# Optimization experiments

Measured on AMD Instinct MI355X. Metric: run time of the kernel, lower is better.

Reference implementation:

```python
import jax, jax.numpy as jnp
import numpy as np

HID = 1024
HEADS = 16
HEAD_DIM = HID // HEADS


def setup_inputs() -> dict:
    key = jax.random.key(0)
    ks = jax.random.split(key, 12)
    B, S = 4, 2048
    scale = 0.02
    return {
        "query": jax.random.normal(ks[0], (B, S, HID), jnp.float32),
        "key": jax.random.normal(ks[1], (B, S, HID), jnp.float32),
        "value": jax.random.normal(ks[2], (B, S, HID), jnp.float32),
        "wq": jax.random.normal(ks[3], (HID, HID), jnp.float32) * scale,
        "bq": jnp.zeros((HID,), jnp.float32),
        "wk": jax.random.normal(ks[4], (HID, HID), jnp.float32) * scale,
        "bk": jnp.zeros((HID,), jnp.float32),
        "wv": jax.random.normal(ks[5], (HID, HID), jnp.float32) * scale,
        "bv": jnp.zeros((HID,), jnp.float32),
        "wf": jax.random.normal(ks[6], (HID, HID), jnp.float32) * scale,
        "bf": jnp.zeros((HID,), jnp.float32),
    }


def reference(query, key, value, wq, bq, wk, bk, wv, bv, wf, bf):
    B, S, _ = query.shape
    # torch Linear: y = x @ W.T + b
    Q = (query @ wq.T + bq).reshape(B, S, HEADS, HEAD_DIM).transpose(0, 2, 1, 3)
    K = (key @ wk.T + bk).reshape(B, S, HEADS, HEAD_DIM).transpose(0, 2, 1, 3)
    V = (value @ wv.T + bv).reshape(B, S, HEADS, HEAD_DIM).transpose(0, 2, 1, 3)
    scale = jnp.sqrt(jnp.float32(HEAD_DIM))
    energy = jnp.einsum('bhqd,bhkd->bhqk', Q, K) / scale  # [B,H,S,S]
    attention = jax.nn.softmax(energy, axis=-1)  # dropout p=0 -> identity
    x = jnp.einsum('bhqk,bhkd->bhqd', attention, V)
    x = x.transpose(0, 2, 1, 3).reshape(B, S, HID)
    return x @ wf.T + bf
```

## Files before the change

kernel.cpp:

```cpp
#include <hip/hip_runtime.h>
#include <stdint.h>

#define SEQ 2048
#define HIDDEN 1024
#define NHEADS 16
#define HDIM 64
#define MTOT 8192

#define C1SCALE 0.1803368801111437f

typedef __bf16 bf16x8 __attribute__((ext_vector_type(8)));
typedef unsigned short u16x8 __attribute__((ext_vector_type(8)));
typedef short s16x4 __attribute__((ext_vector_type(4)));
typedef unsigned int u32x4 __attribute__((ext_vector_type(4)));
typedef float f32x4 __attribute__((ext_vector_type(4)));

#define GAS __attribute__((address_space(1)))
#define LAS __attribute__((address_space(3)))

__device__ __forceinline__ unsigned short bf16_rne(float f) {
  union { float f; unsigned int u; } v; v.f = f;
  return (unsigned short)((v.u + 0x7fffu + ((v.u >> 16) & 1u)) >> 16);
}

__device__ __forceinline__ unsigned int pk2(float lo, float hi) {
  unsigned int a = __builtin_bit_cast(unsigned int, hi) + 0x8000u;
  unsigned int b = __builtin_bit_cast(unsigned int, lo) + 0x8000u;
  return __builtin_amdgcn_perm(a, b, 0x07060302u);
}

__device__ __forceinline__ s16x4 pack4_bf16(float a, float b, float c, float d) {
  s16x4 r;
  r[0] = (short)bf16_rne(a); r[1] = (short)bf16_rne(b);
  r[2] = (short)bf16_rne(c); r[3] = (short)bf16_rne(d);
  return r;
}

__device__ __forceinline__ void gload_lds16(const unsigned short* g, unsigned short* l) {
  __builtin_amdgcn_global_load_lds((GAS void*)(unsigned short*)g, (LAS void*)l, 16, 0, 0);
}

__global__ __launch_bounds__(256) void cvt3(const float* __restrict__ a,
                                            const float* __restrict__ b,
                                            const float* __restrict__ c,
                                            unsigned short* __restrict__ out,
                                            int perSeg) {
  const int seg = blockIdx.y;
  const float* in = seg == 0 ? a : (seg == 1 ? b : c);
  int i = blockIdx.x * 256 + threadIdx.x;
  float4 v = ((const float4*)in)[i];
  ushort4 o;
  o.x = bf16_rne(v.x); o.y = bf16_rne(v.y);
  o.z = bf16_rne(v.z); o.w = bf16_rne(v.w);
  ((ushort4*)(out + (size_t)seg * perSeg))[i] = o;
}

__global__ __launch_bounds__(256) void cvt4(const float* __restrict__ a,
                                            const float* __restrict__ b,
                                            const float* __restrict__ c,
                                            const float* __restrict__ d,
                                            unsigned short* __restrict__ out,
                                            int perSeg) {
  const int seg = blockIdx.y;
  const float* in = seg == 0 ? a : (seg == 1 ? b : (seg == 2 ? c : d));
  const float sc = (seg == 0) ? C1SCALE : 1.0f;
  int i = blockIdx.x * 256 + threadIdx.x;
  float4 v = ((const float4*)in)[i];
  ushort4 o;
  o.x = bf16_rne(v.x * sc); o.y = bf16_rne(v.y * sc);
  o.z = bf16_rne(v.z * sc); o.w = bf16_rne(v.w * sc);
  ((ushort4*)(out + (size_t)seg * perSeg))[i] = o;
}

__global__ __launch_bounds__(256) void gemm_qkv(const unsigned short* __restrict__ Xq,
                                                const unsigned short* __restrict__ Xk,
                                                const unsigned short* __restrict__ Xv,
                                                const unsigned short* __restrict__ W,
                                                const float* __restrict__ bq,
                                                const float* __restrict__ bk,
                                                const float* __restrict__ bv,
                                                unsigned short* __restrict__ Qb,
                                                unsigned short* __restrict__ Kb,
                                                unsigned short* __restrict__ Vb) {
  __shared__ unsigned short As[128 * 32];
  __shared__ unsigned short Bs[128 * 32];
  const int tid = threadIdx.x;
  const int lane = tid & 63, w = tid >> 6;
  const int quad = lane >> 4, ln = lane & 15;
  const int wm = w & 1, wn = w >> 1;
  const int mBase = blockIdx.y * 128, nBase = blockIdx.x * 128;
  const int seg = blockIdx.x >> 3;
  const unsigned short* A = seg == 0 ? Xq : (seg == 1 ? Xk : Xv);
  const float* bias = seg == 0 ? bq : (seg == 1 ? bk : bv);
  const float bscale = seg == 0 ? C1SCALE : 1.0f;
  unsigned short* outp = seg == 0 ? Qb : (seg == 1 ? Kb : Vb);
  const int K = HIDDEN;

  f32x4 acc[4][4];
  f32x4 zero = {0.f, 0.f, 0.f, 0.f};
#pragma unroll
  for (int i = 0; i < 4; i++)
#pragma unroll
    for (int j = 0; j < 4; j++) acc[i][j] = zero;

  const int e0 = tid * 8;
  const int e1 = (256 + tid) * 8;
  const int r0 = e0 >> 5, c0 = e0 & 31;
  const int r1 = e1 >> 5, c1 = e1 & 31;
  const unsigned short* Ap0 = A + (size_t)(mBase + r0) * K + c0;
  const unsigned short* Ap1 = A + (size_t)(mBase + r1) * K + c1;
  const unsigned short* Wp0 = W + (size_t)(nBase + r0) * K + c0;
  const unsigned short* Wp1 = W + (size_t)(nBase + r1) * K + c1;

  for (int k0 = 0; k0 < K; k0 += 32) {
    gload_lds16(Ap0 + k0, &As[e0]);
    gload_lds16(Ap1 + k0, &As[e1]);
    gload_lds16(Wp0 + k0, &Bs[e0]);
    gload_lds16(Wp1 + k0, &Bs[e1]);
    __syncthreads();
    u16x8 af[4], bfr[4];
#pragma unroll
    for (int mi = 0; mi < 4; mi++)
      af[mi] = *(const u16x8*)&As[(wm * 64 + mi * 16 + ln) * 32 + quad * 8];
#pragma unroll
    for (int ni = 0; ni < 4; ni++)
      bfr[ni] = *(const u16x8*)&Bs[(wn * 64 + ni * 16 + ln) * 32 + quad * 8];
#pragma unroll
    for (int mi = 0; mi < 4; mi++)
#pragma unroll
      for (int ni = 0; ni < 4; ni++)
        acc[mi][ni] = __builtin_amdgcn_mfma_f32_16x16x32_bf16(
            __builtin_bit_cast(bf16x8, af[mi]), __builtin_bit_cast(bf16x8, bfr[ni]),
            acc[mi][ni], 0, 0, 0);
    __syncthreads();
  }

#pragma unroll
  for (int ni = 0; ni < 4; ni++) {
    const int colg = nBase + wn * 64 + ni * 16 + ln;
    const int col = colg & 1023;
    const float bvv = bias[col] * bscale;
#pragma unroll
    for (int mi = 0; mi < 4; mi++) {
      const int row = mBase + wm * 64 + mi * 16 + quad * 4;
#pragma unroll
      for (int r = 0; r < 4; r++)
        outp[(size_t)(row + r) * HIDDEN + col] = bf16_rne(acc[mi][ni][r] + bvv);
    }
  }
}

__global__ __launch_bounds__(256) void gemm_f(const unsigned short* __restrict__ A,
                                              const unsigned short* __restrict__ W,
                                              const float* __restrict__ bias,
                                              float* __restrict__ Cv) {
  __shared__ unsigned short As[128 * 32];
  __shared__ unsigned short Bs[128 * 32];
  const int tid = threadIdx.x;
  const int lane = tid & 63, w = tid >> 6;
  const int quad = lane >> 4, ln = lane & 15;
  const int wm = w & 1, wn = w >> 1;
  const int mBase = blockIdx.y * 128, nBase = blockIdx.x * 128;
  const int K = HIDDEN, N = HIDDEN;

  f32x4 acc[4][4];
  f32x4 zero = {0.f, 0.f, 0.f, 0.f};
#pragma unroll
  for (int i = 0; i < 4; i++)
#pragma unroll
    for (int j = 0; j < 4; j++) acc[i][j] = zero;

  const int e0 = tid * 8;
  const int e1 = (256 + tid) * 8;
  const int r0 = e0 >> 5, c0 = e0 & 31;
  const int r1 = e1 >> 5, c1 = e1 & 31;
  const unsigned short* Ap0 = A + (size_t)(mBase + r0) * K + c0;
  const unsigned short* Ap1 = A + (size_t)(mBase + r1) * K + c1;
  const unsigned short* Wp0 = W + (size_t)(nBase + r0) * K + c0;
  const unsigned short* Wp1 = W + (size_t)(nBase + r1) * K + c1;

  for (int k0 = 0; k0 < K; k0 += 32) {
    gload_lds16(Ap0 + k0, &As[e0]);
    gload_lds16(Ap1 + k0, &As[e1]);
    gload_lds16(Wp0 + k0, &Bs[e0]);
    gload_lds16(Wp1 + k0, &Bs[e1]);
    __syncthreads();
    u16x8 af[4], bfr[4];
#pragma unroll
    for (int mi = 0; mi < 4; mi++)
      af[mi] = *(const u16x8*)&As[(wm * 64 + mi * 16 + ln) * 32 + quad * 8];
#pragma unroll
    for (int ni = 0; ni < 4; ni++)
      bfr[ni] = *(const u16x8*)&Bs[(wn * 64 + ni * 16 + ln) * 32 + quad * 8];
#pragma unroll
    for (int mi = 0; mi < 4; mi++)
#pragma unroll
      for (int ni = 0; ni < 4; ni++)
        acc[mi][ni] = __builtin_amdgcn_mfma_f32_16x16x32_bf16(
            __builtin_bit_cast(bf16x8, af[mi]), __builtin_bit_cast(bf16x8, bfr[ni]),
            acc[mi][ni], 0, 0, 0);
    __syncthreads();
  }

#pragma unroll
  for (int ni = 0; ni < 4; ni++) {
    const int col = nBase + wn * 64 + ni * 16 + ln;
    const float bvv = bias[col];
#pragma unroll
    for (int mi = 0; mi < 4; mi++) {
      const int row = mBase + wm * 64 + mi * 16 + quad * 4;
#pragma unroll
      for (int r = 0; r < 4; r++)
        Cv[(size_t)(row + r) * N + col] = acc[mi][ni][r] + bvv;
    }
  }
}

__global__ __launch_bounds__(256) void transpose_v(const unsigned short* __restrict__ Vb,
                                                   unsigned short* __restrict__ Vt) {
  __shared__ unsigned short L[128 * 90];
  const int t = blockIdx.x;
  const int bh = t >> 4, kt = t & 15;
  const int b = bh >> 4, h = bh & 15;
  const int tid = threadIdx.x;
  {
    const int key = tid >> 1, hf = tid & 1;
    const unsigned short* src =
        Vb + ((size_t)(b * SEQ + kt * 128 + key)) * HIDDEN + h * HDIM + hf * 32;
    u16x8 a0 = *(const u16x8*)(src);
    u16x8 a1 = *(const u16x8*)(src + 8);
    u16x8 a2 = *(const u16x8*)(src + 16);
    u16x8 a3 = *(const u16x8*)(src + 24);
    unsigned short* dst = &L[key * 90 + hf * 32];
    *(u16x8*)(dst) = a0;
    *(u16x8*)(dst + 8) = a1;
    *(u16x8*)(dst + 16) = a2;
    *(u16x8*)(dst + 24) = a3;
  }
  __syncthreads();
  const int lane = tid & 63, w = tid >> 6;
  const int quad = lane >> 4, ln = lane & 15;
  unsigned short* out = Vt + (size_t)t * 8192;
#pragma unroll
  for (int gg = 0; gg < 4; gg++) {
    const int f = w * 4 + gg;
    const int g = f >> 2, mtd = f & 3;
    u16x8 v;
#pragma unroll
    for (int j = 0; j < 8; j++) {
      const int key = g * 32 + (j >> 2) * 16 + quad * 4 + (j & 3);
      v[j] = L[key * 90 + mtd * 16 + ln];
    }
    *(u16x8*)(out + f * 512 + lane * 8) = v;
  }
}

__global__ __launch_bounds__(256, 4) void attn8(const unsigned short* __restrict__ Q,
                                                const unsigned short* __restrict__ K,
                                                const unsigned short* __restrict__ Vt,
                                                unsigned short* __restrict__ X) {
  __shared__ unsigned short Ks[2][128 * 64];
  const int tid = threadIdx.x, lane = tid & 63, w = tid >> 6;
  const int quad = lane >> 4, ln = lane & 15;
  const int bh = blockIdx.x, b = bh >> 4, h = bh & 15;
  const size_t base = (size_t)b * SEQ * HIDDEN + (size_t)h * HDIM;
  const unsigned short* Qh = Q + base;
  const unsigned short* Kh = K + base;
  const unsigned short* vtile = Vt + (size_t)bh * 16 * 8192;
  const int qw = blockIdx.y * 128 + w * 32;

  const int kr0 = tid >> 3, kcb = tid & 7;
  const unsigned short* ksrc = Kh + (size_t)kr0 * HIDDEN + ((kcb ^ (kr0 & 7)) * 8);

  const int krd0 = ln * 64 + ((quad ^ (ln & 7)) * 8);
  const int krd1 = ln * 64 + (((4 | quad) ^ (ln & 7)) * 8);

  u16x8 qf[2][2];
#pragma unroll
  for (int nt = 0; nt < 2; nt++)
#pragma unroll
    for (int kk2 = 0; kk2 < 2; kk2++)
      qf[nt][kk2] = *(const u16x8*)(Qh + (size_t)(qw + nt * 16 + ln) * HIDDEN + kk2 * 32 + quad * 8);

  f32x4 o[4][2];
  f32x4 zero = {0.f, 0.f, 0.f, 0.f};
#pragma unroll
  for (int mtd = 0; mtd < 4; mtd++)
#pragma unroll
    for (int nt = 0; nt < 2; nt++) o[mtd][nt] = zero;
  f32x4 l2[2] = {zero, zero};

  u16x8 onesf;
#pragma unroll
  for (int j = 0; j < 8; j++) onesf[j] = 0x3F80;

  {
    unsigned short* kd = &Ks[0][tid * 8];
    gload_lds16(ksrc, kd);
    gload_lds16(ksrc + 32 * HIDDEN, kd + 2048);
    gload_lds16(ksrc + 64 * HIDDEN, kd + 4096);
    gload_lds16(ksrc + 96 * HIDDEN, kd + 6144);
  }

  for (int kt = 0; kt < 16; ++kt) {
    __syncthreads();
    const unsigned short* kb = &Ks[kt & 1][0];
    const unsigned short* vt = vtile + kt * 8192;
#pragma unroll
    for (int g = 0; g < 4; g++) {
      u16x8 vp[4];
#pragma unroll
      for (int mtd = 0; mtd < 4; mtd++)
        vp[mtd] = *(const u16x8*)(vt + (g * 4 + mtd) * 512 + lane * 8);
      if (g == 3 && kt < 15) {
        const unsigned short* ks = ksrc + (size_t)(kt + 1) * (128 * HIDDEN);
        unsigned short* kd = &Ks[(kt + 1) & 1][tid * 8];
        gload_lds16(ks, kd);
        gload_lds16(ks + 32 * HIDDEN, kd + 2048);
        gload_lds16(ks + 64 * HIDDEN, kd + 4096);
        gload_lds16(ks + 96 * HIDDEN, kd + 6144);
      }
      u32x4 P[2];
#pragma unroll
      for (int half = 0; half < 2; half++) {
        const int mt = 2 * g + half;
        const u16x8 kf0 = *(const u16x8*)&kb[mt * 1024 + krd0];
        const u16x8 kf1 = *(const u16x8*)&kb[mt * 1024 + krd1];
        f32x4 s0 = zero, s1 = zero;
        __builtin_amdgcn_s_setprio(1);
        s0 = __builtin_amdgcn_mfma_f32_16x16x32_bf16(
            __builtin_bit_cast(bf16x8, kf0), __builtin_bit_cast(bf16x8, qf[0][0]), s0, 0, 0, 0);
        s0 = __builtin_amdgcn_mfma_f32_16x16x32_bf16(
            __builtin_bit_cast(bf16x8, kf1), __builtin_bit_cast(bf16x8, qf[0][1]), s0, 0, 0, 0);
        s1 = __builtin_amdgcn_mfma_f32_16x16x32_bf16(
            __builtin_bit_cast(bf16x8, kf0), __builtin_bit_cast(bf16x8, qf[1][0]), s1, 0, 0, 0);
        s1 = __builtin_amdgcn_mfma_f32_16x16x32_bf16(
            __builtin_bit_cast(bf16x8, kf1), __builtin_bit_cast(bf16x8, qf[1][1]), s1, 0, 0, 0);
        __builtin_amdgcn_s_setprio(0);
        float e0[4], e1[4];
#pragma unroll
        for (int r = 0; r < 4; r++) {
          e0[r] = __builtin_exp2f(s0[r]);
          e1[r] = __builtin_exp2f(s1[r]);
        }
        if (half == 0) {
          P[0][0] = pk2(e0[0], e0[1]); P[0][1] = pk2(e0[2], e0[3]);
          P[1][0] = pk2(e1[0], e1[1]); P[1][1] = pk2(e1[2], e1[3]);
        } else {
          P[0][2] = pk2(e0[0], e0[1]); P[0][3] = pk2(e0[2], e0[3]);
          P[1][2] = pk2(e1[0], e1[1]); P[1][3] = pk2(e1[2], e1[3]);
        }
      }
      __builtin_amdgcn_s_setprio(1);
#pragma unroll
      for (int nt = 0; nt < 2; nt++) {
        bf16x8 pb = __builtin_bit_cast(bf16x8, P[nt]);
        l2[nt] = __builtin_amdgcn_mfma_f32_16x16x32_bf16(
            __builtin_bit_cast(bf16x8, onesf), pb, l2[nt], 0, 0, 0);
#pragma unroll
        for (int mtd = 0; mtd < 4; mtd++)
          o[mtd][nt] = __builtin_amdgcn_mfma_f32_16x16x32_bf16(
              __builtin_bit_cast(bf16x8, vp[mtd]), pb, o[mtd][nt], 0, 0, 0);
      }
      __builtin_amdgcn_s_setprio(0);
    }
  }

  float inv[2];
#pragma unroll
  for (int nt = 0; nt < 2; nt++) inv[nt] = 1.0f / l2[nt][0];

#pragma unroll
  for (int nt = 0; nt < 2; nt++) {
    unsigned short* dst = X + (size_t)(b * SEQ + qw + nt * 16 + ln) * HIDDEN + h * HDIM;
#pragma unroll
    for (int mtd = 0; mtd < 4; mtd++) {
      s16x4 ov = pack4_bf16(o[mtd][nt][0] * inv[nt], o[mtd][nt][1] * inv[nt],
                            o[mtd][nt][2] * inv[nt], o[mtd][nt][3] * inv[nt]);
      *(s16x4*)(dst + mtd * 16 + quad * 4) = ov;
    }
  }
}

extern "C" void kernel_launch(void* const* d_in, const int* in_sizes, int n_in,
                              void* d_out, int out_size, void* d_ws, size_t ws_size,
                              hipStream_t stream) {
  const float* q_in = (const float*)d_in[0];
  const float* k_in = (const float*)d_in[1];
  const float* v_in = (const float*)d_in[2];
  const float* wq = (const float*)d_in[3];
  const float* bq = (const float*)d_in[4];
  const float* wk = (const float*)d_in[5];
  const float* bk = (const float*)d_in[6];
  const float* wv = (const float*)d_in[7];
  const float* bv = (const float*)d_in[8];
  const float* wf = (const float*)d_in[9];
  const float* bfb = (const float*)d_in[10];

  const size_t NX = (size_t)MTOT * HIDDEN;
  const size_t NW = (size_t)HIDDEN * HIDDEN;
  unsigned short* A = (unsigned short*)d_ws;
  unsigned short* Bx = A + NX;
  unsigned short* C = Bx + NX;
  unsigned short* W4 = C + NX;
  unsigned short* Qb = W4 + 4 * NW;
  unsigned short* Kb = Qb + NX;
  unsigned short* Vb = Kb + NX;

  cvt3<<<dim3(NX / 1024, 3), 256, 0, stream>>>(q_in, k_in, v_in, A, (int)NX);
  cvt4<<<dim3(NW / 1024, 4), 256, 0, stream>>>(wq, wk, wv, wf, W4, (int)NW);

  gemm_qkv<<<dim3(24, MTOT / 128), 256, 0, stream>>>(A, Bx, C, W4, bq, bk, bv, Qb, Kb, Vb);
  transpose_v<<<1024, 256, 0, stream>>>(Vb, Bx);
  attn8<<<dim3(NHEADS * 4, SEQ / 128), 256, 0, stream>>>(Qb, Kb, Bx, C);
  gemm_f<<<dim3(8, MTOT / 128), 256, 0, stream>>>(C, W4 + 3 * NW, bfb, (float*)d_out);
}
```

Before: 369.8 us.

## Fuse V transpose into QKV GEMM epilogue and remap block tiles

The QKV GEMM now writes the V projection directly in the tiled, transposed layout that the attention kernel expects, which removes the separate transpose_v kernel and its extra round trip through global memory. Both GEMMs also remap block indices in a swizzled order, aiming to improve L2 reuse across concurrently running blocks. Float-to-bf16 packing now uses the hardware v_cvt_pk_bf16_f32 instruction in place of manual rounding. The fused epilogue has to match the old transpose layout exactly, and the packing rounding mode may differ slightly from the old pk2.

Measured after the change: 364.3 us. Within noise of the previous version (-1.5%).

```diff
diff --git a/kernel.cpp b/kernel.cpp
--- a/kernel.cpp
+++ b/kernel.cpp
@@ -23,16 +23,9 @@
   return (unsigned short)((v.u + 0x7fffu + ((v.u >> 16) & 1u)) >> 16);
 }
 
-__device__ __forceinline__ unsigned int pk2(float lo, float hi) {
-  unsigned int a = __builtin_bit_cast(unsigned int, hi) + 0x8000u;
-  unsigned int b = __builtin_bit_cast(unsigned int, lo) + 0x8000u;
-  return __builtin_amdgcn_perm(a, b, 0x07060302u);
-}
-
-__device__ __forceinline__ s16x4 pack4_bf16(float a, float b, float c, float d) {
-  s16x4 r;
-  r[0] = (short)bf16_rne(a); r[1] = (short)bf16_rne(b);
-  r[2] = (short)bf16_rne(c); r[3] = (short)bf16_rne(d);
+__device__ __forceinline__ unsigned int pkcvt(float lo, float hi) {
+  unsigned int r;
+  asm("v_cvt_pk_bf16_f32 %0, %1, %2" : "=v"(r) : "v"(lo), "v"(hi));
   return r;
 }
 
@@ -81,19 +74,21 @@
                                                 const float* __restrict__ bv,
                                                 unsigned short* __restrict__ Qb,
                                                 unsigned short* __restrict__ Kb,
-                                                unsigned short* __restrict__ Vb) {
+                                                unsigned short* __restrict__ Vt) {
   __shared__ unsigned short As[128 * 32];
   __shared__ unsigned short Bs[128 * 32];
   const int tid = threadIdx.x;
   const int lane = tid & 63, w = tid >> 6;
   const int quad = lane >> 4, ln = lane & 15;
   const int wm = w & 1, wn = w >> 1;
-  const int mBase = blockIdx.y * 128, nBase = blockIdx.x * 128;
-  const int seg = blockIdx.x >> 3;
+  const int flat = blockIdx.y * 24 + blockIdx.x;
+  const int wid = (flat & 7) * 192 + (flat >> 3);
+  const int mIdx = wid / 24, nIdx = wid % 24;
+  const int mBase = mIdx * 128, nBase = (nIdx & 7) * 128;
+  const int seg = nIdx >> 3;
   const unsigned short* A = seg == 0 ? Xq : (seg == 1 ? Xk : Xv);
   const float* bias = seg == 0 ? bq : (seg == 1 ? bk : bv);
   const float bscale = seg == 0 ? C1SCALE : 1.0f;
-  unsigned short* outp = seg == 0 ? Qb : (seg == 1 ? Kb : Vb);
   const int K = HIDDEN;
 
   f32x4 acc[4][4];
@@ -109,8 +104,8 @@
   const int r1 = e1 >> 5, c1 = e1 & 31;
   const unsigned short* Ap0 = A + (size_t)(mBase + r0) * K + c0;
   const unsigned short* Ap1 = A + (size_t)(mBase + r1) * K + c1;
-  const unsigned short* Wp0 = W + (size_t)(nBase + r0) * K + c0;
-  const unsigned short* Wp1 = W + (size_t)(nBase + r1) * K + c1;
+  const unsigned short* Wp0 = W + (size_t)(seg * HIDDEN + nBase + r0) * K + c0;
+  const unsigned short* Wp1 = W + (size_t)(seg * HIDDEN + nBase + r1) * K + c1;
 
   for (int k0 = 0; k0 < K; k0 += 32) {
     gload_lds16(Ap0 + k0, &As[e0]);
@@ -135,17 +130,39 @@
     __syncthreads();
   }
 
-#pragma unroll
-  for (int ni = 0; ni < 4; ni++) {
-    const int colg = nBase + wn * 64 + ni * 16 + ln;
-    const int col = colg & 1023;
-    const float bvv = bias[col] * bscale;
-#pragma unroll
-    for (int mi = 0; mi < 4; mi++) {
-      const int row = mBase + wm * 64 + mi * 16 + quad * 4;
-#pragma unroll
-      for (int r = 0; r < 4; r++)
-        outp[(size_t)(row + r) * HIDDEN + col] = bf16_rne(acc[mi][ni][r] + bvv);
+  if (seg < 2) {
+    unsigned short* outp = seg == 0 ? Qb : Kb;
+#pragma unroll
+    for (int ni = 0; ni < 4; ni++) {
+      const int col = nBase + wn * 64 + ni * 16 + ln;
+      const float bvv = bias[col] * bscale;
+#pragma unroll
+      for (int mi = 0; mi < 4; mi++) {
+        const int row = mBase + wm * 64 + mi * 16 + quad * 4;
+#pragma unroll
+        for (int r = 0; r < 4; r++)
+          outp[(size_t)(row + r) * HIDDEN + col] = bf16_rne(acc[mi][ni][r] + bvv);
+      }
+    }
+  } else {
+    const int b = mBase >> 11;
+    const int kt = (mBase & 2047) >> 7;
+    const int h = (nBase >> 6) + wn;
+    unsigned short* tb = Vt + (((size_t)(b * NHEADS + h) * 16 + kt) * 8192) + lane * 8;
+#pragma unroll
+    for (int ni = 0; ni < 4; ni++) {
+      const int col = nBase + wn * 64 + ni * 16 + ln;
+      const float bvv = bias[col];
+#pragma unroll
+      for (int p = 0; p < 2; p++) {
+        const int f = (wm * 2 + p) * 4 + ni;
+        u32x4 ov;
+        ov[0] = pkcvt(acc[2 * p][ni][0] + bvv, acc[2 * p][ni][1] + bvv);
+        ov[1] = pkcvt(acc[2 * p][ni][2] + bvv, acc[2 * p][ni][3] + bvv);
+        ov[2] = pkcvt(acc[2 * p + 1][ni][0] + bvv, acc[2 * p + 1][ni][1] + bvv);
+        ov[3] = pkcvt(acc[2 * p + 1][ni][2] + bvv, acc[2 * p + 1][ni][3] + bvv);
+        *(u32x4*)(tb + f * 512) = ov;
+      }
     }
   }
 }
@@ -160,7 +177,9 @@
   const int lane = tid & 63, w = tid >> 6;
   const int quad = lane >> 4, ln = lane & 15;
   const int wm = w & 1, wn = w >> 1;
-  const int mBase = blockIdx.y * 128, nBase = blockIdx.x * 128;
+  const int flat = blockIdx.y * 8 + blockIdx.x;
+  const int wid = (flat & 7) * 64 + (flat >> 3);
+  const int mBase = (wid >> 3) * 128, nBase = (wid & 7) * 128;
   const int K = HIDDEN, N = HIDDEN;
 
   f32x4 acc[4][4];
@@ -216,46 +235,7 @@
   }
 }
 
-__global__ __launch_bounds__(256) void transpose_v(const unsigned short* __restrict__ Vb,
-                                                   unsigned short* __restrict__ Vt) {
-  __shared__ unsigned short L[128 * 90];
-  const int t = blockIdx.x;
-  const int bh = t >> 4, kt = t & 15;
-  const int b = bh >> 4, h = bh & 15;
-  const int tid = threadIdx.x;
-  {
-    const int key = tid >> 1, hf = tid & 1;
-    const unsigned short* src =
-        Vb + ((size_t)(b * SEQ + kt * 128 + key)) * HIDDEN + h * HDIM + hf * 32;
-    u16x8 a0 = *(const u16x8*)(src);
-    u16x8 a1 = *(const u16x8*)(src + 8);
-    u16x8 a2 = *(const u16x8*)(src + 16);
-    u16x8 a3 = *(const u16x8*)(src + 24);
-    unsigned short* dst = &L[key * 90 + hf * 32];
-    *(u16x8*)(dst) = a0;
-    *(u16x8*)(dst + 8) = a1;
-    *(u16x8*)(dst + 16) = a2;
-    *(u16x8*)(dst + 24) = a3;
-  }
-  __syncthreads();
-  const int lane = tid & 63, w = tid >> 6;
-  const int quad = lane >> 4, ln = lane & 15;
-  unsigned short* out = Vt + (size_t)t * 8192;
-#pragma unroll
-  for (int gg = 0; gg < 4; gg++) {
-    const int f = w * 4 + gg;
-    const int g = f >> 2, mtd = f & 3;
-    u16x8 v;
-#pragma unroll
-    for (int j = 0; j < 8; j++) {
-      const int key = g * 32 + (j >> 2) * 16 + quad * 4 + (j & 3);
-      v[j] = L[key * 90 + mtd * 16 + ln];
-    }
-    *(u16x8*)(out + f * 512 + lane * 8) = v;
-  }
-}
-
-__global__ __launch_bounds__(256, 4) void attn8(const unsigned short* __restrict__ Q,
+__global__ __launch_bounds__(256, 4) void attn9(const unsigned short* __restrict__ Q,
                                                 const unsigned short* __restrict__ K,
                                                 const unsigned short* __restrict__ Vt,
                                                 unsigned short* __restrict__ X) {
@@ -344,11 +324,11 @@
           e1[r] = __builtin_exp2f(s1[r]);
         }
         if (half == 0) {
-          P[0][0] = pk2(e0[0], e0[1]); P[0][1] = pk2(e0[2], e0[3]);
-          P[1][0] = pk2(e1[0], e1[1]); P[1][1] = pk2(e1[2], e1[3]);
+          P[0][0] = pkcvt(e0[0], e0[1]); P[0][1] = pkcvt(e0[2], e0[3]);
+          P[1][0] = pkcvt(e1[0], e1[1]); P[1][1] = pkcvt(e1[2], e1[3]);
         } else {
-          P[0][2] = pk2(e0[0], e0[1]); P[0][3] = pk2(e0[2], e0[3]);
-          P[1][2] = pk2(e1[0], e1[1]); P[1][3] = pk2(e1[2], e1[3]);
+          P[0][2] = pkcvt(e0[0], e0[1]); P[0][3] = pkcvt(e0[2], e0[3]);
+          P[1][2] = pkcvt(e1[0], e1[1]); P[1][3] = pkcvt(e1[2], e1[3]);
         }
       }
       __builtin_amdgcn_s_setprio(1);
@@ -375,9 +355,10 @@
     unsigned short* dst = X + (size_t)(b * SEQ + qw + nt * 16 + ln) * HIDDEN + h * HDIM;
 #pragma unroll
     for (int mtd = 0; mtd < 4; mtd++) {
-      s16x4 ov = pack4_bf16(o[mtd][nt][0] * inv[nt], o[mtd][nt][1] * inv[nt],
-                            o[mtd][nt][2] * inv[nt], o[mtd][nt][3] * inv[nt]);
-      *(s16x4*)(dst + mtd * 16 + quad * 4) = ov;
+      uint2 ov;
+      ov.x = pkcvt(o[mtd][nt][0] * inv[nt], o[mtd][nt][1] * inv[nt]);
+      ov.y = pkcvt(o[mtd][nt][2] * inv[nt], o[mtd][nt][3] * inv[nt]);
+      *(uint2*)(dst + mtd * 16 + quad * 4) = ov;
     }
   }
 }
@@ -405,13 +386,12 @@
   unsigned short* W4 = C + NX;
   unsigned short* Qb = W4 + 4 * NW;
   unsigned short* Kb = Qb + NX;
-  unsigned short* Vb = Kb + NX;
+  unsigned short* Vtb = Kb + NX;
 
   cvt3<<<dim3(NX / 1024, 3), 256, 0, stream>>>(q_in, k_in, v_in, A, (int)NX);
   cvt4<<<dim3(NW / 1024, 4), 256, 0, stream>>>(wq, wk, wv, wf, W4, (int)NW);
 
-  gemm_qkv<<<dim3(24, MTOT / 128), 256, 0, stream>>>(A, Bx, C, W4, bq, bk, bv, Qb, Kb, Vb);
-  transpose_v<<<1024, 256, 0, stream>>>(Vb, Bx);
-  attn8<<<dim3(NHEADS * 4, SEQ / 128), 256, 0, stream>>>(Qb, Kb, Bx, C);
+  gemm_qkv<<<dim3(24, MTOT / 128), 256, 0, stream>>>(A, Bx, C, W4, bq, bk, bv, Qb, Kb, Vtb);
+  attn9<<<dim3(NHEADS * 4, SEQ / 128), 256, 0, stream>>>(Qb, Kb, Vtb, C);
   gemm_f<<<dim3(8, MTOT / 128), 256, 0, stream>>>(C, W4 + 3 * NW, bfb, (float*)d_out);
 }
```
